# Kernel tuning notes

Hardware: AMD Instinct MI355X
Metric: run time of the kernel (lower is better)

## Reference

```python
import jax, jax.numpy as jnp
import numpy as np

N_NODES = 50000
N_EDGES = 800000
N_LABEL_EDGES = 200000
IN_CH = 256
HID = 64
OUT_CH = 64


def gcn_conv(x, W, b, edge_index, n_nodes):
    """PyG GCNConv: symmetric-normalized aggregation with self-loops.
    out[col] = sum_row norm(row,col) * (x @ W)[row] + b
    """
    xw = x @ W  # [N, out]
    loops = jnp.arange(n_nodes, dtype=edge_index.dtype)
    row = jnp.concatenate([edge_index[0], loops])  # source
    col = jnp.concatenate([edge_index[1], loops])  # target
    deg = jax.ops.segment_sum(jnp.ones_like(col, dtype=xw.dtype), col, num_segments=n_nodes)
    dis = jnp.where(deg > 0, jax.lax.rsqrt(deg), 0.0)
    norm = dis[row] * dis[col]  # [E+N]
    out = jax.ops.segment_sum(xw[row] * norm[:, None], col, num_segments=n_nodes)
    return out + b


def setup_inputs() -> dict:
    key = jax.random.key(0)
    k0, k1, k2, k3, k4 = jax.random.split(key, 5)
    x = jax.random.normal(k0, (N_NODES, IN_CH), dtype=jnp.float32)
    edge_index = jax.random.randint(k1, (2, N_EDGES), 0, N_NODES, dtype=jnp.int32)
    edge_label_index = jax.random.randint(k2, (2, N_LABEL_EDGES), 0, N_NODES, dtype=jnp.int32)
    W1 = jax.random.normal(k3, (IN_CH, HID), dtype=jnp.float32) * (1.0 / np.sqrt(IN_CH))
    b1 = jnp.zeros((HID,), dtype=jnp.float32)
    W2 = jax.random.normal(k4, (HID, OUT_CH), dtype=jnp.float32) * (1.0 / np.sqrt(HID))
    b2 = jnp.zeros((OUT_CH,), dtype=jnp.float32)
    return {"x": x, "edge_index": edge_index, "edge_label_index": edge_label_index,
            "W1": W1, "b1": b1, "W2": W2, "b2": b2}


def reference(x, edge_index, edge_label_index, W1, b1, W2, b2):
    n = x.shape[0]
    # encode: two GCNConv layers with ReLU between
    h = jax.nn.relu(gcn_conv(x, W1, b1, edge_index, n))
    z = gcn_conv(h, W2, b2, edge_index, n)
    # decode: gather node pairs, elementwise multiply, sum over features
    src, dst = edge_label_index[0], edge_label_index[1]
    return jnp.sum(z[src] * z[dst], axis=1)  # [N_LABEL_EDGES]
```

## Files before the change

kernel.cpp:

```cpp
#include <hip/hip_runtime.h>
#include <hip/hip_bf16.h>


constexpr int NC = 512;
constexpr int NBPAD = 256;
constexpr int BSHIFT = 8;

__device__ __forceinline__ unsigned short f2bf(float f) {
    unsigned u = __float_as_uint(f);
    return (unsigned short)((u + 0x7FFF + ((u >> 16) & 1)) >> 16);
}
__device__ __forceinline__ float bflo(unsigned u) { return __uint_as_float(u << 16); }
__device__ __forceinline__ float bfhi(unsigned u) { return __uint_as_float(u & 0xFFFF0000u); }

__device__ __forceinline__ void bfacc8(float* acc, uint4 q) {
    acc[0] += bflo(q.x); acc[1] += bfhi(q.x);
    acc[2] += bflo(q.y); acc[3] += bfhi(q.y);
    acc[4] += bflo(q.z); acc[5] += bfhi(q.z);
    acc[6] += bflo(q.w); acc[7] += bfhi(q.w);
}

__global__ __launch_bounds__(256) void hist_kernel(const int* __restrict__ col,
                                                   int* __restrict__ hist,
                                                   int* __restrict__ bsums, int E, int CE) {
    __shared__ int hl[NBPAD];
    const int t = threadIdx.x, c = blockIdx.x;
    hl[t] = 0;
    __syncthreads();
    const int s = c * CE, e = min(E, s + CE);
    for (int i = s + t; i < e; i += 256) atomicAdd(&hl[col[i] >> BSHIFT], 1);
    __syncthreads();
    const int v = hl[t];
    hist[t * NC + c] = v;
    if (v) atomicAdd(&bsums[t], v);
}

__global__ __launch_bounds__(256) void rowscan_kernel(int* __restrict__ hist,
                                                      const int* __restrict__ bsums) {
    __shared__ int sb[256];
    __shared__ int sc[256];
    const int t = threadIdx.x, b = blockIdx.x;
    sb[t] = bsums[t];
    __syncthreads();
    for (int off = 1; off < 256; off <<= 1) {
        int u = (t >= off) ? sb[t - off] : 0;
        __syncthreads();
        sb[t] += u;
        __syncthreads();
    }
    const int base = (b == 0) ? 0 : sb[b - 1];
    const int i0 = b * NC + 2 * t;
    const int a0 = hist[i0], a1 = hist[i0 + 1];
    const int ps = a0 + a1;
    sc[t] = ps;
    __syncthreads();
    for (int off = 1; off < 256; off <<= 1) {
        int u = (t >= off) ? sc[t - off] : 0;
        __syncthreads();
        sc[t] += u;
        __syncthreads();
    }
    const int excl = sc[t] - ps;
    hist[i0] = base + excl;
    hist[i0 + 1] = base + excl + a0;
}

__global__ __launch_bounds__(256) void reorder_kernel(const int* __restrict__ row,
                                                      const int* __restrict__ col,
                                                      const int* __restrict__ hist,
                                                      int2* __restrict__ part, int E, int CE) {
    __shared__ int cur[NBPAD];
    const int t = threadIdx.x, c = blockIdx.x;
    cur[t] = hist[t * NC + c];
    __syncthreads();
    const int s = c * CE, e = min(E, s + CE);
    for (int i = s + t; i < e; i += 256) {
        const int r = row[i], cl = col[i];
        const int p = atomicAdd(&cur[cl >> BSHIFT], 1);
        part[p] = make_int2(r, cl);
    }
}

__global__ __launch_bounds__(256) void bucket_csr_kernel(const int2* __restrict__ part,
                                                         const int* __restrict__ hist,
                                                         int* __restrict__ csr,
                                                         int* __restrict__ offs,
                                                         float* __restrict__ dis,
                                                         int N, int E, int nbk) {
    __shared__ int cnt[256];
    __shared__ int sc[256];
    const int t = threadIdx.x, b = blockIdx.x;
    const int base = b << BSHIFT;
    const int bstart = hist[b * NC];
    const int bend = (b + 1 < NBPAD) ? hist[(b + 1) * NC] : E;
    const int m = bend - bstart;
    cnt[t] = 0;
    __syncthreads();
    for (int i = t; i < m; i += 256) atomicAdd(&cnt[part[bstart + i].y - base], 1);
    __syncthreads();
    const int v = cnt[t];
    sc[t] = v;
    __syncthreads();
    for (int off = 1; off < 256; off <<= 1) {
        int u = (t >= off) ? sc[t - off] : 0;
        __syncthreads();
        sc[t] += u;
        __syncthreads();
    }
    const int excl = sc[t] - v;
    const int node = base + t;
    if (node < N) {
        offs[node] = bstart + excl;
        dis[node] = rsqrtf((float)(v + 1));
    }
    sc[t] = excl;
    __syncthreads();
    for (int i = t; i < m; i += 256) {
        const int2 ec = part[bstart + i];
        const int p = atomicAdd(&sc[ec.y - base], 1);
        csr[bstart + p] = ec.x;
    }
    if (b == nbk - 1 && t == 0) offs[N] = E;
}

template <int K>
__global__ __launch_bounds__(256) void gemm_tile(const float* __restrict__ X,
                                                 const float* __restrict__ W,
                                                 const float* __restrict__ rowscale,
                                                 unsigned short* __restrict__ Y, int nrows) {
    __shared__ float sX[64 * 64];
    __shared__ float sW[64 * 64];
    const int tid = threadIdx.x;
    const int tx = tid & 15;
    const int ty = tid >> 4;
    const int rowbase = blockIdx.x * 64;

    float acc[16];
    #pragma unroll
    for (int i = 0; i < 16; ++i) acc[i] = 0.f;

    const int lr = tid & 63;
    const int lq = tid >> 6;
    int grow = rowbase + lr;
    if (grow >= nrows) grow = nrows - 1;
    const float* xrow = X + (long)grow * K;

    for (int kc = 0; kc < K; kc += 64) {
        if (kc) __syncthreads();
        #pragma unroll
        for (int i = 0; i < 4; ++i) {
            const int o = tid * 4 + i * 1024;
            *(float4*)&sW[o] = *(const float4*)&W[(long)kc * 64 + o];
        }
        #pragma unroll
        for (int t = 0; t < 4; ++t) {
            const int k = lq * 16 + t * 4;
            const float4 v = *(const float4*)&xrow[kc + k];
            sX[(k + 0) * 64 + lr] = v.x;
            sX[(k + 1) * 64 + lr] = v.y;
            sX[(k + 2) * 64 + lr] = v.z;
            sX[(k + 3) * 64 + lr] = v.w;
        }
        __syncthreads();
        #pragma unroll 4
        for (int k = 0; k < 64; ++k) {
            const float4 xv = *(const float4*)&sX[k * 64 + ty * 4];
            const float4 wv = *(const float4*)&sW[k * 64 + tx * 4];
            acc[0]  = fmaf(xv.x, wv.x, acc[0]);
            acc[1]  = fmaf(xv.x, wv.y, acc[1]);
            acc[2]  = fmaf(xv.x, wv.z, acc[2]);
            acc[3]  = fmaf(xv.x, wv.w, acc[3]);
            acc[4]  = fmaf(xv.y, wv.x, acc[4]);
            acc[5]  = fmaf(xv.y, wv.y, acc[5]);
            acc[6]  = fmaf(xv.y, wv.z, acc[6]);
            acc[7]  = fmaf(xv.y, wv.w, acc[7]);
            acc[8]  = fmaf(xv.z, wv.x, acc[8]);
            acc[9]  = fmaf(xv.z, wv.y, acc[9]);
            acc[10] = fmaf(xv.z, wv.z, acc[10]);
            acc[11] = fmaf(xv.z, wv.w, acc[11]);
            acc[12] = fmaf(xv.w, wv.x, acc[12]);
            acc[13] = fmaf(xv.w, wv.y, acc[13]);
            acc[14] = fmaf(xv.w, wv.z, acc[14]);
            acc[15] = fmaf(xv.w, wv.w, acc[15]);
        }
    }

    #pragma unroll
    for (int i = 0; i < 4; ++i) {
        const int orow = rowbase + ty * 4 + i;
        if (orow < nrows) {
            const float d = rowscale[orow];
            ushort4 ov;
            ov.x = f2bf(d * acc[i * 4 + 0]);
            ov.y = f2bf(d * acc[i * 4 + 1]);
            ov.z = f2bf(d * acc[i * 4 + 2]);
            ov.w = f2bf(d * acc[i * 4 + 3]);
            *(ushort4*)&Y[(long)orow * 64 + tx * 4] = ov;
        }
    }
}

template <bool RELU, bool OUT_BF16>
__global__ __launch_bounds__(256) void agg_kernel(const unsigned short* __restrict__ xs,
                                                  const int* __restrict__ csr,
                                                  const int* __restrict__ offs,
                                                  const float* __restrict__ dis,
                                                  const float* __restrict__ bias,
                                                  void* __restrict__ out, int n) {
    __shared__ int sidx[4][64];
    const int wv = threadIdx.x >> 6;
    const int lane = threadIdx.x & 63;
    const int grp = lane >> 3;
    const int fl = lane & 7;
    const int i = blockIdx.x * 4 + wv;
    if (i >= n) return;
    float acc[8];
    #pragma unroll
    for (int j = 0; j < 8; ++j) acc[j] = 0.f;
    if (grp == 0)
        bfacc8(acc, *(const uint4*)&xs[(long)i * 64 + fl * 8]);
    const int s = offs[i];
    const int e = offs[i + 1];
    for (int jb = s; jb < e; jb += 64) {
        const int nb = min(64, e - jb);
        if (lane < nb) sidx[wv][lane] = csr[jb + lane];
        int u = grp;
        for (; u + 8 < nb; u += 16) {
            const int r0 = sidx[wv][u];
            const int r1 = sidx[wv][u + 8];
            const uint4 q0 = *(const uint4*)&xs[(long)r0 * 64 + fl * 8];
            const uint4 q1 = *(const uint4*)&xs[(long)r1 * 64 + fl * 8];
            bfacc8(acc, q0);
            bfacc8(acc, q1);
        }
        for (; u < nb; u += 8) {
            const int r0 = sidx[wv][u];
            bfacc8(acc, *(const uint4*)&xs[(long)r0 * 64 + fl * 8]);
        }
    }
    #pragma unroll
    for (int j = 0; j < 8; ++j) {
        acc[j] += __shfl_xor(acc[j], 8);
        acc[j] += __shfl_xor(acc[j], 16);
        acc[j] += __shfl_xor(acc[j], 32);
    }
    if (grp == 0) {
        const float di = dis[i];
        const float4 b0 = *(const float4*)&bias[fl * 8 + 0];
        const float4 b4 = *(const float4*)&bias[fl * 8 + 4];
        float o[8];
        o[0] = fmaf(acc[0], di, b0.x); o[1] = fmaf(acc[1], di, b0.y);
        o[2] = fmaf(acc[2], di, b0.z); o[3] = fmaf(acc[3], di, b0.w);
        o[4] = fmaf(acc[4], di, b4.x); o[5] = fmaf(acc[5], di, b4.y);
        o[6] = fmaf(acc[6], di, b4.z); o[7] = fmaf(acc[7], di, b4.w);
        if (RELU) {
            #pragma unroll
            for (int j = 0; j < 8; ++j) o[j] = fmaxf(o[j], 0.f);
        }
        if (OUT_BF16) {
            uint4 q;
            q.x = (unsigned)f2bf(o[0]) | ((unsigned)f2bf(o[1]) << 16);
            q.y = (unsigned)f2bf(o[2]) | ((unsigned)f2bf(o[3]) << 16);
            q.z = (unsigned)f2bf(o[4]) | ((unsigned)f2bf(o[5]) << 16);
            q.w = (unsigned)f2bf(o[6]) | ((unsigned)f2bf(o[7]) << 16);
            *(uint4*)&((unsigned short*)out)[(long)i * 64 + fl * 8] = q;
        } else {
            float* op = (float*)out + (long)i * 64 + fl * 8;
            *(float4*)&op[0] = make_float4(o[0], o[1], o[2], o[3]);
            *(float4*)&op[4] = make_float4(o[4], o[5], o[6], o[7]);
        }
    }
}

__global__ __launch_bounds__(256) void decode_kernel(const unsigned short* __restrict__ z,
                                                     const int* __restrict__ src,
                                                     const int* __restrict__ dst,
                                                     float* __restrict__ out, int L) {
    const int t = blockIdx.x * 256 + threadIdx.x;
    const int e = t >> 3;
    const int fl = t & 7;
    if (e >= L) return;
    const int s = src[e];
    const int d = dst[e];
    const uint4 qa = *(const uint4*)&z[(long)s * 64 + fl * 8];
    const uint4 qb = *(const uint4*)&z[(long)d * 64 + fl * 8];
    float p = bflo(qa.x) * bflo(qb.x) + bfhi(qa.x) * bfhi(qb.x)
            + bflo(qa.y) * bflo(qb.y) + bfhi(qa.y) * bfhi(qb.y)
            + bflo(qa.z) * bflo(qb.z) + bfhi(qa.z) * bfhi(qb.z)
            + bflo(qa.w) * bflo(qb.w) + bfhi(qa.w) * bfhi(qb.w);
    p += __shfl_xor(p, 4); p += __shfl_xor(p, 2); p += __shfl_xor(p, 1);
    if (fl == 0) out[e] = p;
}

extern "C" void kernel_launch(void* const* d_in, const int* in_sizes, int n_in,
                              void* d_out, int out_size, void* d_ws, size_t ws_size,
                              hipStream_t stream) {
    const float* x   = (const float*)d_in[0];
    const int*   ei  = (const int*)d_in[1];
    const int*   eli = (const int*)d_in[2];
    const float* W1  = (const float*)d_in[3];
    const float* b1  = (const float*)d_in[4];
    const float* W2  = (const float*)d_in[5];
    const float* b2  = (const float*)d_in[6];
    float* out = (float*)d_out;

    const int N = in_sizes[0] / 256;
    const int E = in_sizes[1] / 2;
    const int L = in_sizes[2] / 2;
    const int* row = ei;
    const int* col = ei + E;
    const int* src = eli;
    const int* dst = eli + L;

    char* w = (char*)d_ws;
    unsigned short* xs = (unsigned short*)w;  w += (size_t)N * 64 * 2;
    float* h   = (float*)w;  w += (size_t)N * 64 * 4;
    unsigned short* z = (unsigned short*)w;  w += (size_t)N * 64 * 2;
    int*   csr = (int*)w;    w += (size_t)E * 4;
    int*   offs = (int*)w;   w += (size_t)(N + 1) * 4;
    float* dis = (float*)w;  w += (size_t)N * 4;
    int2*  part = (int2*)w;  w += (size_t)E * 8;
    int*  hist  = (int*)h;
    int*  bsums = hist + NBPAD * NC;

    const int CE = (E + NC - 1) / NC;
    const int nbk = (N + (1 << BSHIFT) - 1) >> BSHIFT;

    hipMemsetAsync(bsums, 0, NBPAD * sizeof(int), stream);
    hist_kernel<<<NC, 256, 0, stream>>>(col, hist, bsums, E, CE);
    rowscan_kernel<<<NBPAD, 256, 0, stream>>>(hist, bsums);
    reorder_kernel<<<NC, 256, 0, stream>>>(row, col, hist, part, E, CE);
    bucket_csr_kernel<<<nbk, 256, 0, stream>>>(part, hist, csr, offs, dis, N, E, nbk);

    gemm_tile<256><<<(N + 63) / 64, 256, 0, stream>>>(x, W1, dis, xs, N);
    agg_kernel<true, false><<<(N + 3) / 4, 256, 0, stream>>>(xs, csr, offs, dis, b1, h, N);
    gemm_tile<64><<<(N + 63) / 64, 256, 0, stream>>>(h, W2, dis, xs, N);
    agg_kernel<false, true><<<(N + 3) / 4, 256, 0, stream>>>(xs, csr, offs, dis, b2, z, N);
    decode_kernel<<<(L * 8 + 255) / 256, 256, 0, stream>>>(z, src, dst, out, L);
}
```

Measured before the change: 228.2 us.

## Aggregate directly from bucket-partitioned edges with LDS atomics, dropping CSR build

Removes the per-node CSR construction pass, so the bucket kernel now only computes degrees. Aggregation becomes agg_fused: each block owns a 64-node slice and scans its 256-node bucket's edge list, keeping edges for its slice. It gathers source rows and accumulates them with float atomics into a padded shared-memory tile. Histogram and offset storage move to separate column-major and bucket-major buffers, and the scan base is now computed with a reduction. The trade-off is that each edge record is read four times, far fewer blocks are launched, feature accumulation uses shared-memory atomics, and summation order becomes nondeterministic.

New measurement: 865.3 us. +279.3%, slower.

```diff
diff --git a/kernel.cpp b/kernel.cpp
--- a/kernel.cpp
+++ b/kernel.cpp
@@ -13,15 +13,8 @@
 __device__ __forceinline__ float bflo(unsigned u) { return __uint_as_float(u << 16); }
 __device__ __forceinline__ float bfhi(unsigned u) { return __uint_as_float(u & 0xFFFF0000u); }
 
-__device__ __forceinline__ void bfacc8(float* acc, uint4 q) {
-    acc[0] += bflo(q.x); acc[1] += bfhi(q.x);
-    acc[2] += bflo(q.y); acc[3] += bfhi(q.y);
-    acc[4] += bflo(q.z); acc[5] += bfhi(q.z);
-    acc[6] += bflo(q.w); acc[7] += bfhi(q.w);
-}
-
 __global__ __launch_bounds__(256) void hist_kernel(const int* __restrict__ col,
-                                                   int* __restrict__ hist,
+                                                   int* __restrict__ histCM,
                                                    int* __restrict__ bsums, int E, int CE) {
     __shared__ int hl[NBPAD];
     const int t = threadIdx.x, c = blockIdx.x;
@@ -31,26 +24,25 @@
     for (int i = s + t; i < e; i += 256) atomicAdd(&hl[col[i] >> BSHIFT], 1);
     __syncthreads();
     const int v = hl[t];
-    hist[t * NC + c] = v;
+    histCM[c * NBPAD + t] = v;
     if (v) atomicAdd(&bsums[t], v);
 }
 
-__global__ __launch_bounds__(256) void rowscan_kernel(int* __restrict__ hist,
-                                                      const int* __restrict__ bsums) {
-    __shared__ int sb[256];
+__global__ __launch_bounds__(256) void rowscan_kernel(const int* __restrict__ histCM,
+                                                      const int* __restrict__ bsums,
+                                                      int* __restrict__ offsBM) {
+    __shared__ int red[256];
     __shared__ int sc[256];
     const int t = threadIdx.x, b = blockIdx.x;
-    sb[t] = bsums[t];
-    __syncthreads();
-    for (int off = 1; off < 256; off <<= 1) {
-        int u = (t >= off) ? sb[t - off] : 0;
+    red[t] = (t < b) ? bsums[t] : 0;
+    __syncthreads();
+    for (int off = 128; off > 0; off >>= 1) {
+        if (t < off) red[t] += red[t + off];
         __syncthreads();
-        sb[t] += u;
-        __syncthreads();
-    }
-    const int base = (b == 0) ? 0 : sb[b - 1];
-    const int i0 = b * NC + 2 * t;
-    const int a0 = hist[i0], a1 = hist[i0 + 1];
+    }
+    const int base = red[0];
+    const int a0 = histCM[(2 * t) * NBPAD + b];
+    const int a1 = histCM[(2 * t + 1) * NBPAD + b];
     const int ps = a0 + a1;
     sc[t] = ps;
     __syncthreads();
@@ -61,17 +53,17 @@
         __syncthreads();
     }
     const int excl = sc[t] - ps;
-    hist[i0] = base + excl;
-    hist[i0 + 1] = base + excl + a0;
+    offsBM[b * NC + 2 * t] = base + excl;
+    offsBM[b * NC + 2 * t + 1] = base + excl + a0;
 }
 
 __global__ __launch_bounds__(256) void reorder_kernel(const int* __restrict__ row,
                                                       const int* __restrict__ col,
-                                                      const int* __restrict__ hist,
+                                                      const int* __restrict__ offsBM,
                                                       int2* __restrict__ part, int E, int CE) {
     __shared__ int cur[NBPAD];
     const int t = threadIdx.x, c = blockIdx.x;
-    cur[t] = hist[t * NC + c];
+    cur[t] = offsBM[t * NC + c];
     __syncthreads();
     const int s = c * CE, e = min(E, s + CE);
     for (int i = s + t; i < e; i += 256) {
@@ -81,46 +73,21 @@
     }
 }
 
-__global__ __launch_bounds__(256) void bucket_csr_kernel(const int2* __restrict__ part,
-                                                         const int* __restrict__ hist,
-                                                         int* __restrict__ csr,
-                                                         int* __restrict__ offs,
+__global__ __launch_bounds__(256) void bucket_deg_kernel(const int2* __restrict__ part,
+                                                         const int* __restrict__ offsBM,
                                                          float* __restrict__ dis,
-                                                         int N, int E, int nbk) {
+                                                         int N, int E) {
     __shared__ int cnt[256];
-    __shared__ int sc[256];
     const int t = threadIdx.x, b = blockIdx.x;
     const int base = b << BSHIFT;
-    const int bstart = hist[b * NC];
-    const int bend = (b + 1 < NBPAD) ? hist[(b + 1) * NC] : E;
-    const int m = bend - bstart;
+    const int bstart = offsBM[b * NC];
+    const int bend = (b + 1 < NBPAD) ? offsBM[(b + 1) * NC] : E;
     cnt[t] = 0;
     __syncthreads();
-    for (int i = t; i < m; i += 256) atomicAdd(&cnt[part[bstart + i].y - base], 1);
-    __syncthreads();
-    const int v = cnt[t];
-    sc[t] = v;
-    __syncthreads();
-    for (int off = 1; off < 256; off <<= 1) {
-        int u = (t >= off) ? sc[t - off] : 0;
-        __syncthreads();
-        sc[t] += u;
-        __syncthreads();
-    }
-    const int excl = sc[t] - v;
+    for (int i = bstart + t; i < bend; i += 256) atomicAdd(&cnt[part[i].y - base], 1);
+    __syncthreads();
     const int node = base + t;
-    if (node < N) {
-        offs[node] = bstart + excl;
-        dis[node] = rsqrtf((float)(v + 1));
-    }
-    sc[t] = excl;
-    __syncthreads();
-    for (int i = t; i < m; i += 256) {
-        const int2 ec = part[bstart + i];
-        const int p = atomicAdd(&sc[ec.y - base], 1);
-        csr[bstart + p] = ec.x;
-    }
-    if (b == nbk - 1 && t == 0) offs[N] = E;
+    if (node < N) dis[node] = rsqrtf((float)(cnt[t] + 1));
 }
 
 template <int K>
@@ -201,73 +168,77 @@
 }
 
 template <bool RELU, bool OUT_BF16>
-__global__ __launch_bounds__(256) void agg_kernel(const unsigned short* __restrict__ xs,
-                                                  const int* __restrict__ csr,
-                                                  const int* __restrict__ offs,
-                                                  const float* __restrict__ dis,
-                                                  const float* __restrict__ bias,
-                                                  void* __restrict__ out, int n) {
-    __shared__ int sidx[4][64];
-    const int wv = threadIdx.x >> 6;
-    const int lane = threadIdx.x & 63;
-    const int grp = lane >> 3;
-    const int fl = lane & 7;
-    const int i = blockIdx.x * 4 + wv;
-    if (i >= n) return;
-    float acc[8];
-    #pragma unroll
-    for (int j = 0; j < 8; ++j) acc[j] = 0.f;
-    if (grp == 0)
-        bfacc8(acc, *(const uint4*)&xs[(long)i * 64 + fl * 8]);
-    const int s = offs[i];
-    const int e = offs[i + 1];
-    for (int jb = s; jb < e; jb += 64) {
-        const int nb = min(64, e - jb);
-        if (lane < nb) sidx[wv][lane] = csr[jb + lane];
-        int u = grp;
-        for (; u + 8 < nb; u += 16) {
-            const int r0 = sidx[wv][u];
-            const int r1 = sidx[wv][u + 8];
-            const uint4 q0 = *(const uint4*)&xs[(long)r0 * 64 + fl * 8];
-            const uint4 q1 = *(const uint4*)&xs[(long)r1 * 64 + fl * 8];
-            bfacc8(acc, q0);
-            bfacc8(acc, q1);
-        }
-        for (; u < nb; u += 8) {
-            const int r0 = sidx[wv][u];
-            bfacc8(acc, *(const uint4*)&xs[(long)r0 * 64 + fl * 8]);
-        }
-    }
-    #pragma unroll
-    for (int j = 0; j < 8; ++j) {
-        acc[j] += __shfl_xor(acc[j], 8);
-        acc[j] += __shfl_xor(acc[j], 16);
-        acc[j] += __shfl_xor(acc[j], 32);
-    }
-    if (grp == 0) {
-        const float di = dis[i];
-        const float4 b0 = *(const float4*)&bias[fl * 8 + 0];
-        const float4 b4 = *(const float4*)&bias[fl * 8 + 4];
-        float o[8];
-        o[0] = fmaf(acc[0], di, b0.x); o[1] = fmaf(acc[1], di, b0.y);
-        o[2] = fmaf(acc[2], di, b0.z); o[3] = fmaf(acc[3], di, b0.w);
-        o[4] = fmaf(acc[4], di, b4.x); o[5] = fmaf(acc[5], di, b4.y);
-        o[6] = fmaf(acc[6], di, b4.z); o[7] = fmaf(acc[7], di, b4.w);
-        if (RELU) {
-            #pragma unroll
-            for (int j = 0; j < 8; ++j) o[j] = fmaxf(o[j], 0.f);
+__global__ __launch_bounds__(256) void agg_fused(const unsigned short* __restrict__ xs,
+                                                 const int2* __restrict__ part,
+                                                 const int* __restrict__ offsBM,
+                                                 const float* __restrict__ dis,
+                                                 const float* __restrict__ bias,
+                                                 void* __restrict__ out, int N, int E) {
+    __shared__ float accum[64 * 65];
+    const int t = threadIdx.x;
+    const int base = blockIdx.x << 6;
+    const int bkt = blockIdx.x >> 2;
+    const int bstart = offsBM[bkt * NC];
+    const int bend = (bkt + 1 < NBPAD) ? offsBM[(bkt + 1) * NC] : E;
+
+    {
+        const int node = t >> 2, fq = t & 3;
+        const unsigned short* p = &xs[(size_t)(base + node) * 64 + fq * 16];
+        const uint4 q0 = *(const uint4*)p;
+        const uint4 q1 = *(const uint4*)(p + 8);
+        float* a = &accum[node * 65 + fq * 16];
+        a[0] = bflo(q0.x); a[1] = bfhi(q0.x); a[2] = bflo(q0.y); a[3] = bfhi(q0.y);
+        a[4] = bflo(q0.z); a[5] = bfhi(q0.z); a[6] = bflo(q0.w); a[7] = bfhi(q0.w);
+        a[8] = bflo(q1.x); a[9] = bfhi(q1.x); a[10] = bflo(q1.y); a[11] = bfhi(q1.y);
+        a[12] = bflo(q1.z); a[13] = bfhi(q1.z); a[14] = bflo(q1.w); a[15] = bfhi(q1.w);
+    }
+    __syncthreads();
+
+    const int g = t >> 3;
+    const int fl = t & 7;
+    for (int i = bstart + g; i < bend; i += 32) {
+        const int2 ec = part[i];
+        const unsigned d = (unsigned)(ec.y - base);
+        if (d < 64u) {
+            const uint4 q = *(const uint4*)&xs[(size_t)ec.x * 64 + fl * 8];
+            float* a = &accum[d * 65 + fl * 8];
+            atomicAdd(&a[0], bflo(q.x)); atomicAdd(&a[1], bfhi(q.x));
+            atomicAdd(&a[2], bflo(q.y)); atomicAdd(&a[3], bfhi(q.y));
+            atomicAdd(&a[4], bflo(q.z)); atomicAdd(&a[5], bfhi(q.z));
+            atomicAdd(&a[6], bflo(q.w)); atomicAdd(&a[7], bfhi(q.w));
+        }
+    }
+    __syncthreads();
+
+    const int node = t >> 2, fq = t & 3;
+    if (base + node < N) {
+        const float di = dis[base + node];
+        const float* a = &accum[node * 65 + fq * 16];
+        float o[16];
+        #pragma unroll
+        for (int j = 0; j < 16; ++j) {
+            o[j] = fmaf(a[j], di, bias[fq * 16 + j]);
+            if (RELU) o[j] = fmaxf(o[j], 0.f);
         }
         if (OUT_BF16) {
-            uint4 q;
-            q.x = (unsigned)f2bf(o[0]) | ((unsigned)f2bf(o[1]) << 16);
-            q.y = (unsigned)f2bf(o[2]) | ((unsigned)f2bf(o[3]) << 16);
-            q.z = (unsigned)f2bf(o[4]) | ((unsigned)f2bf(o[5]) << 16);
-            q.w = (unsigned)f2bf(o[6]) | ((unsigned)f2bf(o[7]) << 16);
-            *(uint4*)&((unsigned short*)out)[(long)i * 64 + fl * 8] = q;
+            uint4 q0, q1;
+            q0.x = (unsigned)f2bf(o[0]) | ((unsigned)f2bf(o[1]) << 16);
+            q0.y = (unsigned)f2bf(o[2]) | ((unsigned)f2bf(o[3]) << 16);
+            q0.z = (unsigned)f2bf(o[4]) | ((unsigned)f2bf(o[5]) << 16);
+            q0.w = (unsigned)f2bf(o[6]) | ((unsigned)f2bf(o[7]) << 16);
+            q1.x = (unsigned)f2bf(o[8]) | ((unsigned)f2bf(o[9]) << 16);
+            q1.y = (unsigned)f2bf(o[10]) | ((unsigned)f2bf(o[11]) << 16);
+            q1.z = (unsigned)f2bf(o[12]) | ((unsigned)f2bf(o[13]) << 16);
+            q1.w = (unsigned)f2bf(o[14]) | ((unsigned)f2bf(o[15]) << 16);
+            unsigned short* op = (unsigned short*)out + (size_t)(base + node) * 64 + fq * 16;
+            *(uint4*)&op[0] = q0;
+            *(uint4*)&op[8] = q1;
         } else {
-            float* op = (float*)out + (long)i * 64 + fl * 8;
+            float* op = (float*)out + (size_t)(base + node) * 64 + fq * 16;
             *(float4*)&op[0] = make_float4(o[0], o[1], o[2], o[3]);
             *(float4*)&op[4] = make_float4(o[4], o[5], o[6], o[7]);
+            *(float4*)&op[8] = make_float4(o[8], o[9], o[10], o[11]);
+            *(float4*)&op[12] = make_float4(o[12], o[13], o[14], o[15]);
         }
     }
 }
@@ -316,25 +287,25 @@
     unsigned short* xs = (unsigned short*)w;  w += (size_t)N * 64 * 2;
     float* h   = (float*)w;  w += (size_t)N * 64 * 4;
     unsigned short* z = (unsigned short*)w;  w += (size_t)N * 64 * 2;
-    int*   csr = (int*)w;    w += (size_t)E * 4;
-    int*   offs = (int*)w;   w += (size_t)(N + 1) * 4;
-    float* dis = (float*)w;  w += (size_t)N * 4;
     int2*  part = (int2*)w;  w += (size_t)E * 8;
-    int*  hist  = (int*)h;
-    int*  bsums = hist + NBPAD * NC;
+    float* dis  = (float*)w; w += (size_t)((N + 63) & ~63) * 4;
+    int* histCM = (int*)w;   w += (size_t)NC * NBPAD * 4;
+    int* offsBM = (int*)w;   w += (size_t)NBPAD * NC * 4;
+    int* bsums  = (int*)w;   w += NBPAD * 4;
 
     const int CE = (E + NC - 1) / NC;
     const int nbk = (N + (1 << BSHIFT) - 1) >> BSHIFT;
+    const int nslice = (N + 63) >> 6;
 
     hipMemsetAsync(bsums, 0, NBPAD * sizeof(int), stream);
-    hist_kernel<<<NC, 256, 0, stream>>>(col, hist, bsums, E, CE);
-    rowscan_kernel<<<NBPAD, 256, 0, stream>>>(hist, bsums);
-    reorder_kernel<<<NC, 256, 0, stream>>>(row, col, hist, part, E, CE);
-    bucket_csr_kernel<<<nbk, 256, 0, stream>>>(part, hist, csr, offs, dis, N, E, nbk);
+    hist_kernel<<<NC, 256, 0, stream>>>(col, histCM, bsums, E, CE);
+    rowscan_kernel<<<NBPAD, 256, 0, stream>>>(histCM, bsums, offsBM);
+    reorder_kernel<<<NC, 256, 0, stream>>>(row, col, offsBM, part, E, CE);
+    bucket_deg_kernel<<<nbk, 256, 0, stream>>>(part, offsBM, dis, N, E);
 
     gemm_tile<256><<<(N + 63) / 64, 256, 0, stream>>>(x, W1, dis, xs, N);
-    agg_kernel<true, false><<<(N + 3) / 4, 256, 0, stream>>>(xs, csr, offs, dis, b1, h, N);
+    agg_fused<true, false><<<nslice, 256, 0, stream>>>(xs, part, offsBM, dis, b1, h, N, E);
     gemm_tile<64><<<(N + 63) / 64, 256, 0, stream>>>(h, W2, dis, xs, N);
-    agg_kernel<false, true><<<(N + 3) / 4, 256, 0, stream>>>(xs, csr, offs, dis, b2, z, N);
+    agg_fused<false, true><<<nslice, 256, 0, stream>>>(xs, part, offsBM, dis, b2, z, N, E);
     decode_kernel<<<(L * 8 + 255) / 256, 256, 0, stream>>>(z, src, dst, out, L);
 }
```
